# Kernel tuning notes

Measured on AMD Instinct MI355X. Metric: run time of the kernel, lower is better.

The kernel has to match this reference:

```python
import jax, jax.numpy as jnp
import numpy as np

B, S, H, UNITS = 32, 2048, 1024, 128

def setup_inputs() -> dict:
    key = jax.random.key(0)
    k1, k2, k3 = jax.random.split(key, 3)
    hidden_states = jax.random.normal(k1, (B, S, H), dtype=jnp.float32)
    # Dense(hidden_size, use_bias=False): weight [H, H]
    w_score = jax.random.normal(k2, (H, H), dtype=jnp.float32) * (1.0 / np.sqrt(H))
    # Dense(units, use_bias=False): weight [2H, units]
    w_out = jax.random.normal(k3, (2 * H, UNITS), dtype=jnp.float32) * (1.0 / np.sqrt(2 * H))
    return {"hidden_states": hidden_states, "w_score": w_score, "w_out": w_out}

def reference(hidden_states, w_score, w_out):
    # dense_score: [B,S,H] @ [H,H] -> [B,S,H]
    dense_score = jnp.einsum('bsh,hk->bsk', hidden_states, w_score)
    h_t = hidden_states[:, -1, :]                       # [B,H] last hidden state
    score = jnp.einsum('bh,bsh->bs', h_t, dense_score)  # attention scores [B,S]
    attn = jax.nn.softmax(score, axis=-1)               # [B,S]
    context = jnp.einsum('bsh,bs->bh', hidden_states, attn)  # [B,H]
    pre = jnp.concatenate([context, h_t], axis=-1)      # [B,2H]
    return jnp.tanh(pre @ w_out)                        # [B,units]
```

## Files before the change

### kernel.cpp

```cpp
#include <hip/hip_runtime.h>
#include <math.h>

#define B_ 32
#define S_ 2048
#define H_ 1024
#define U_ 128

#define OFF_VPART 0u
#define OFF_V     262144u
#define OFF_PM    294912u
#define OFF_PL    299008u
#define OFF_PCTX  303104u
#define OFF_CTX   4497408u
#define OFF_DPART 4530176u

typedef float vfloat4 __attribute__((ext_vector_type(4)));

static __device__ __forceinline__ float4 ntload4(const float* p) {
    vfloat4 v = __builtin_nontemporal_load((const vfloat4*)p);
    return make_float4(v.x, v.y, v.z, v.w);
}

__global__ __launch_bounds__(256) void k_vpart(const float* __restrict__ hid,
                                               const float* __restrict__ W,
                                               float* __restrict__ ws) {
    __shared__ float ht[32][128];
    const int t  = threadIdx.x;
    const int h0 = blockIdx.x * 64;
    const int k0 = blockIdx.y * 128;
    #pragma unroll
    for (int i = 0; i < 4; ++i) {
        int f4 = i * 256 + t;
        int bl = f4 >> 5;
        int k4 = f4 & 31;
        float4 src = *(const float4*)(hid + ((size_t)bl * S_ + (S_ - 1)) * H_ + k0 + k4 * 4);
        *(float4*)&ht[bl][k4 * 4] = src;
    }
    __syncthreads();
    const int hl = t & 63;
    const int g  = t >> 6;
    const int h  = h0 + hl;
    float acc[8];
    #pragma unroll
    for (int i = 0; i < 8; ++i) acc[i] = 0.f;
    const float4* Wr = (const float4*)(W + (size_t)h * H_ + k0);
    for (int k4 = 0; k4 < 32; ++k4) {
        float4 w4 = Wr[k4];
        float wv[4] = {w4.x, w4.y, w4.z, w4.w};
        #pragma unroll
        for (int c = 0; c < 4; ++c) {
            float w = wv[c];
            int kk = k4 * 4 + c;
            #pragma unroll
            for (int bb = 0; bb < 8; ++bb)
                acc[bb] += w * ht[g * 8 + bb][kk];
        }
    }
    float* vpart = ws + OFF_VPART;
    const int kc = blockIdx.y;
    #pragma unroll
    for (int bb = 0; bb < 8; ++bb)
        vpart[((size_t)kc * 32 + (g * 8 + bb)) * H_ + h] = acc[bb];
}

__global__ __launch_bounds__(256) void k_vreduce(float* __restrict__ ws) {
    int e = blockIdx.x * 256 + threadIdx.x;
    const float* vp = ws + OFF_VPART;
    float s = 0.f;
    #pragma unroll
    for (int kc = 0; kc < 8; ++kc) s += vp[kc * 32768 + e];
    ws[OFF_V + e] = s;
}

__global__ __launch_bounds__(256) void k_flash(const float* __restrict__ hid,
                                               float* __restrict__ ws) {
    const int t    = threadIdx.x;
    const int lane = t & 63;
    const int wave = t >> 6;
    const int b    = blockIdx.x >> 5;
    const int wi   = (blockIdx.x & 31) * 4 + wave;
    const int s0   = wi * 16;

    const float* vrow = ws + OFF_V + (size_t)b * H_;
    float4 v4[4], c4[4];
    #pragma unroll
    for (int j = 0; j < 4; ++j) {
        v4[j] = *(const float4*)(vrow + j * 256 + lane * 4);
        c4[j] = make_float4(0.f, 0.f, 0.f, 0.f);
    }
    float m = -INFINITY, l = 0.f;
    const float* base = hid + ((size_t)b * S_ + s0) * H_ + lane * 4;

    for (int r = 0; r < 16; r += 2) {
        const float* r0 = base + (size_t)r * H_;
        const float* r1 = r0 + H_;
        float4 a4[4], b4[4];
        #pragma unroll
        for (int j = 0; j < 4; ++j) a4[j] = ntload4(r0 + j * 256);
        #pragma unroll
        for (int j = 0; j < 4; ++j) b4[j] = ntload4(r1 + j * 256);
        float p0 = 0.f, p1 = 0.f;
        #pragma unroll
        for (int j = 0; j < 4; ++j) {
            p0 += a4[j].x * v4[j].x + a4[j].y * v4[j].y + a4[j].z * v4[j].z + a4[j].w * v4[j].w;
            p1 += b4[j].x * v4[j].x + b4[j].y * v4[j].y + b4[j].z * v4[j].z + b4[j].w * v4[j].w;
        }
        #pragma unroll
        for (int off = 32; off > 0; off >>= 1) {
            p0 += __shfl_xor(p0, off, 64);
            p1 += __shfl_xor(p1, off, 64);
        }
        float pmax = fmaxf(p0, p1);
        if (pmax > m) {
            float alpha = __expf(m - pmax);
            l *= alpha;
            #pragma unroll
            for (int j = 0; j < 4; ++j) {
                c4[j].x *= alpha; c4[j].y *= alpha; c4[j].z *= alpha; c4[j].w *= alpha;
            }
            m = pmax;
        }
        float e0 = __expf(p0 - m), e1 = __expf(p1 - m);
        l += e0 + e1;
        #pragma unroll
        for (int j = 0; j < 4; ++j) {
            c4[j].x += e0 * a4[j].x + e1 * b4[j].x;
            c4[j].y += e0 * a4[j].y + e1 * b4[j].y;
            c4[j].z += e0 * a4[j].z + e1 * b4[j].z;
            c4[j].w += e0 * a4[j].w + e1 * b4[j].w;
        }
    }
    const int pid = b * 128 + wi;
    float* pctx = ws + OFF_PCTX + (size_t)pid * H_;
    #pragma unroll
    for (int j = 0; j < 4; ++j)
        *(float4*)(pctx + j * 256 + lane * 4) = c4[j];
    if (lane == 0) { ws[OFF_PM + pid] = m; ws[OFF_PL + pid] = l; }
}

__global__ __launch_bounds__(256) void k_merge(float* __restrict__ ws) {
    const int cc = blockIdx.x;
    const int b  = blockIdx.y;
    const int t  = threadIdx.x;
    const float* pm = ws + OFF_PM + b * 128;
    const float* pl = ws + OFF_PL + b * 128;
    float M = -INFINITY;
    #pragma unroll 8
    for (int i = 0; i < 128; ++i) M = fmaxf(M, pm[i]);
    float L = 0.f, c = 0.f;
    const float* pctx = ws + OFF_PCTX + (size_t)b * 128 * H_ + cc * 256 + t;
    #pragma unroll 4
    for (int i = 0; i < 128; ++i) {
        float w = __expf(pm[i] - M);
        L += pl[i] * w;
        c += w * pctx[(size_t)i * H_];
    }
    ws[OFF_CTX + (size_t)b * H_ + cc * 256 + t] = c / L;
}

__global__ __launch_bounds__(128) void k_out_part(const float* __restrict__ hid,
                                                  const float* __restrict__ W2,
                                                  float* __restrict__ ws) {
    __shared__ float pre[256];
    const int jc = blockIdx.x;
    const int b  = blockIdx.y;
    const int t  = threadIdx.x;
    #pragma unroll
    for (int i = 0; i < 2; ++i) {
        int idx = t * 2 + i;
        int j = jc * 256 + idx;
        float val = (j < 1024)
            ? ws[OFF_CTX + (size_t)b * H_ + j]
            : hid[((size_t)b * S_ + (S_ - 1)) * H_ + (j - 1024)];
        pre[idx] = val;
    }
    __syncthreads();
    float acc = 0.f;
    const float* w2 = W2 + (size_t)jc * 256 * U_ + t;
    #pragma unroll 8
    for (int jj = 0; jj < 256; ++jj)
        acc += pre[jj] * w2[(size_t)jj * U_];
    ws[OFF_DPART + ((size_t)jc * 32 + b) * U_ + t] = acc;
}

__global__ __launch_bounds__(256) void k_out_final(const float* __restrict__ ws,
                                                   float* __restrict__ out) {
    int idx = blockIdx.x * 256 + threadIdx.x;
    float s = 0.f;
    #pragma unroll
    for (int jc = 0; jc < 8; ++jc) s += ws[OFF_DPART + jc * 4096 + idx];
    out[idx] = tanhf(s);
}

extern "C" void kernel_launch(void* const* d_in, const int* in_sizes, int n_in,
                              void* d_out, int out_size, void* d_ws, size_t ws_size,
                              hipStream_t stream) {
    const float* hid = (const float*)d_in[0];
    const float* W   = (const float*)d_in[1];
    const float* W2  = (const float*)d_in[2];
    float* ws  = (float*)d_ws;
    float* out = (float*)d_out;

    hipLaunchKernelGGL(k_vpart,     dim3(16, 8), dim3(256), 0, stream, hid, W, ws);
    hipLaunchKernelGGL(k_vreduce,   dim3(128),   dim3(256), 0, stream, ws);
    hipLaunchKernelGGL(k_flash,     dim3(1024),  dim3(256), 0, stream, hid, ws);
    hipLaunchKernelGGL(k_merge,     dim3(4, 32), dim3(256), 0, stream, ws);
    hipLaunchKernelGGL(k_out_part,  dim3(8, 32), dim3(128), 0, stream, hid, W2, ws);
    hipLaunchKernelGGL(k_out_final, dim3(16),    dim3(256), 0, stream, ws, out);
}
```

Before: 388.7 us.

## Merge flash partials in-block via LDS and fuse final merge into out_part

Each flash block now combines its four waves' partial softmax states (max, sum, context) through shared memory before writing, so it emits 32 partials per batch instead of 128. The separate merge kernel is removed and its work folded into k_out_part, which combines the 32 partials while building the context part of its input vector. This cuts partial-context write and read traffic by four and drops one kernel launch. In exchange k_flash adds a block barrier and uses 16KB of LDS, and out_part blocks redo the max and weight computation.

```diff
diff --git a/kernel.cpp b/kernel.cpp
--- a/kernel.cpp
+++ b/kernel.cpp
@@ -9,10 +9,9 @@
 #define OFF_VPART 0u
 #define OFF_V     262144u
 #define OFF_PM    294912u
-#define OFF_PL    299008u
-#define OFF_PCTX  303104u
-#define OFF_CTX   4497408u
-#define OFF_DPART 4530176u
+#define OFF_PL    295936u
+#define OFF_PCTX  296960u
+#define OFF_DPART 1345536u
 
 typedef float vfloat4 __attribute__((ext_vector_type(4)));
 
@@ -74,11 +73,14 @@
 
 __global__ __launch_bounds__(256) void k_flash(const float* __restrict__ hid,
                                                float* __restrict__ ws) {
+    __shared__ float sm[4], sl[4];
+    __shared__ __align__(16) float sc[4][1024];
     const int t    = threadIdx.x;
     const int lane = t & 63;
     const int wave = t >> 6;
     const int b    = blockIdx.x >> 5;
-    const int wi   = (blockIdx.x & 31) * 4 + wave;
+    const int blk  = blockIdx.x & 31;
+    const int wi   = blk * 4 + wave;
     const int s0   = wi * 16;
 
     const float* vrow = ws + OFF_V + (size_t)b * H_;
@@ -130,32 +132,28 @@
             c4[j].w += e0 * a4[j].w + e1 * b4[j].w;
         }
     }
-    const int pid = b * 128 + wi;
-    float* pctx = ws + OFF_PCTX + (size_t)pid * H_;
+
+    if (lane == 0) { sm[wave] = m; sl[wave] = l; }
     #pragma unroll
     for (int j = 0; j < 4; ++j)
-        *(float4*)(pctx + j * 256 + lane * 4) = c4[j];
-    if (lane == 0) { ws[OFF_PM + pid] = m; ws[OFF_PL + pid] = l; }
-}
-
-__global__ __launch_bounds__(256) void k_merge(float* __restrict__ ws) {
-    const int cc = blockIdx.x;
-    const int b  = blockIdx.y;
-    const int t  = threadIdx.x;
-    const float* pm = ws + OFF_PM + b * 128;
-    const float* pl = ws + OFF_PL + b * 128;
-    float M = -INFINITY;
-    #pragma unroll 8
-    for (int i = 0; i < 128; ++i) M = fmaxf(M, pm[i]);
-    float L = 0.f, c = 0.f;
-    const float* pctx = ws + OFF_PCTX + (size_t)b * 128 * H_ + cc * 256 + t;
-    #pragma unroll 4
-    for (int i = 0; i < 128; ++i) {
-        float w = __expf(pm[i] - M);
-        L += pl[i] * w;
-        c += w * pctx[(size_t)i * H_];
-    }
-    ws[OFF_CTX + (size_t)b * H_ + cc * 256 + t] = c / L;
+        *(float4*)&sc[wave][j * 256 + lane * 4] = c4[j];
+    __syncthreads();
+
+    float M = fmaxf(fmaxf(sm[0], sm[1]), fmaxf(sm[2], sm[3]));
+    const int col = t * 4;
+    float4 acc = make_float4(0.f, 0.f, 0.f, 0.f);
+    float Lm = 0.f;
+    #pragma unroll
+    for (int w = 0; w < 4; ++w) {
+        float wt = __expf(sm[w] - M);
+        float4 cw = *(const float4*)&sc[w][col];
+        acc.x += wt * cw.x; acc.y += wt * cw.y;
+        acc.z += wt * cw.z; acc.w += wt * cw.w;
+        Lm += wt * sl[w];
+    }
+    const int pid = b * 32 + blk;
+    *(float4*)(ws + OFF_PCTX + (size_t)pid * H_ + col) = acc;
+    if (t == 0) { ws[OFF_PM + pid] = M; ws[OFF_PL + pid] = Lm; }
 }
 
 __global__ __launch_bounds__(128) void k_out_part(const float* __restrict__ hid,
@@ -165,14 +163,31 @@
     const int jc = blockIdx.x;
     const int b  = blockIdx.y;
     const int t  = threadIdx.x;
-    #pragma unroll
-    for (int i = 0; i < 2; ++i) {
-        int idx = t * 2 + i;
-        int j = jc * 256 + idx;
-        float val = (j < 1024)
-            ? ws[OFF_CTX + (size_t)b * H_ + j]
-            : hid[((size_t)b * S_ + (S_ - 1)) * H_ + (j - 1024)];
-        pre[idx] = val;
+    if (jc < 4) {
+        const float* pm = ws + OFF_PM + b * 32;
+        const float* pl = ws + OFF_PL + b * 32;
+        float M = -INFINITY;
+        #pragma unroll
+        for (int i = 0; i < 32; ++i) M = fmaxf(M, pm[i]);
+        float w[32];
+        float L = 0.f;
+        #pragma unroll
+        for (int i = 0; i < 32; ++i) { w[i] = __expf(pm[i] - M); L += w[i] * pl[i]; }
+        float2 acc = make_float2(0.f, 0.f);
+        const float* basep = ws + OFF_PCTX + (size_t)b * 32 * H_ + jc * 256 + t * 2;
+        #pragma unroll
+        for (int i = 0; i < 32; ++i) {
+            float2 cv = *(const float2*)(basep + (size_t)i * H_);
+            acc.x += w[i] * cv.x; acc.y += w[i] * cv.y;
+        }
+        float invL = 1.f / L;
+        pre[t * 2]     = acc.x * invL;
+        pre[t * 2 + 1] = acc.y * invL;
+    } else {
+        const float* hrow = hid + ((size_t)b * S_ + (S_ - 1)) * H_ + (jc - 4) * 256;
+        float2 h2 = *(const float2*)(hrow + t * 2);
+        pre[t * 2]     = h2.x;
+        pre[t * 2 + 1] = h2.y;
     }
     __syncthreads();
     float acc = 0.f;
@@ -204,7 +219,6 @@
     hipLaunchKernelGGL(k_vpart,     dim3(16, 8), dim3(256), 0, stream, hid, W, ws);
     hipLaunchKernelGGL(k_vreduce,   dim3(128),   dim3(256), 0, stream, ws);
     hipLaunchKernelGGL(k_flash,     dim3(1024),  dim3(256), 0, stream, hid, ws);
-    hipLaunchKernelGGL(k_merge,     dim3(4, 32), dim3(256), 0, stream, ws);
     hipLaunchKernelGGL(k_out_part,  dim3(8, 32), dim3(128), 0, stream, hid, W2, ws);
     hipLaunchKernelGGL(k_out_final, dim3(16),    dim3(256), 0, stream, ws, out);
 }
```

Result: faster. 368.9 us (-5.1%).
